# Performance work log

Hardware: AMD Instinct MI355X
Metric: run time of the kernel (lower is better)

The kernel has to match this reference:

```python
import jax, jax.numpy as jnp
import numpy as np

D_IN = 768
D_LATENT = 16384
BATCH = 8192
K = 32


def _xavier(key, shape):
    fan_out, fan_in = shape
    limit = float(np.sqrt(6.0 / (fan_in + fan_out)))
    return jax.random.uniform(key, shape, jnp.float32, -limit, limit)


def setup_inputs() -> dict:
    key = jax.random.key(0)
    k1, k2, k3 = jax.random.split(key, 3)
    x = jax.random.normal(k1, (BATCH, D_IN), dtype=jnp.float32)
    W_enc = _xavier(k2, (D_LATENT, D_IN))   # encoder.weight: [d_latent, d_in]
    W_dec = _xavier(k3, (D_IN, D_LATENT))   # decoder.weight: [d_in, d_latent]
    return {"x": x, "W_enc": W_enc, "W_dec": W_dec, "k": K}


def reference(x, W_enc, W_dec, k):
    # Encoder: Linear (no bias) + ReLU -> z: [B, d_latent]
    z = jax.nn.relu(jnp.einsum('bd,ld->bl', x, W_enc))
    # Per-row top-k mask via scatter of ones at top-k indices
    _, idx = jax.lax.top_k(z, k)                      # idx: [B, k]
    rows = jnp.arange(z.shape[0])[:, None]            # [B, 1]
    mask = jnp.zeros_like(z).at[rows, idx].set(1.0)
    z = z * mask
    # Decoder: Linear (no bias) -> x_hat: [B, d_in]
    x_hat = jnp.einsum('bl,dl->bd', z, W_dec)
    return x_hat, z
```

## Files before the change

kernel.cpp:

```cpp
#include <hip/hip_runtime.h>
#include <hip/hip_bf16.h>
#include <stdint.h>

#define MB 8192
#define NL 16384
#define KD 768
#define TOPK 32
#define CAND_NEED 48
#define TAU 0.70f
#define CAP_MIN 288

typedef short bf16x8 __attribute__((ext_vector_type(8)));
typedef float f32x4 __attribute__((ext_vector_type(4)));
typedef unsigned short ushort_t;

__device__ __forceinline__ short f2bf(float f) {
  unsigned u = __builtin_bit_cast(unsigned, f);
  u = (u + 0x7fffu + ((u >> 16) & 1u)) >> 16;
  return (short)u;
}
__device__ __forceinline__ float bf2f(ushort_t u) {
  return __builtin_bit_cast(float, (unsigned)u << 16);
}

__device__ __forceinline__ void gload16(const ushort_t* g, short* l) {
  __builtin_amdgcn_global_load_lds(
      (const __attribute__((address_space(1))) void*)g,
      (__attribute__((address_space(3))) void*)l, 16, 0, 0);
}

__global__ __launch_bounds__(256) void cvt_bf16(const float* __restrict__ in,
                                                ushort_t* __restrict__ out, int n8) {
  int i = blockIdx.x * 256 + threadIdx.x;
  if (i >= n8) return;
  const float4 v0 = *(const float4*)(in + (size_t)i * 8);
  const float4 v1 = *(const float4*)(in + (size_t)i * 8 + 4);
  bf16x8 p;
  p[0] = f2bf(v0.x); p[1] = f2bf(v0.y); p[2] = f2bf(v0.z); p[3] = f2bf(v0.w);
  p[4] = f2bf(v1.x); p[5] = f2bf(v1.y); p[6] = f2bf(v1.z); p[7] = f2bf(v1.w);
  *(bf16x8*)(out + (size_t)i * 8) = p;
}

__global__ __launch_bounds__(256) void transpose_wdec_pack(const float* __restrict__ W,
                                                           ushort_t* __restrict__ WT) {
  __shared__ float tile[32][33];
  int l0 = blockIdx.x * 32;
  int d0 = blockIdx.y * 32;
  int lx = threadIdx.x;
  for (int i = threadIdx.y; i < 32; i += 8)
    tile[i][lx] = W[(size_t)(d0 + i) * NL + (l0 + lx)];
  __syncthreads();
  int d = d0 + lx;
  int pos = (d < 512) ? ((d & 255) * 2 + (d >> 8)) : d;
  for (int i = threadIdx.y; i < 32; i += 8)
    WT[(size_t)(l0 + i) * KD + pos] = (ushort_t)f2bf(tile[lx][i]);
}

#define GBM 128
#define GBN 128
#define GBK 32
#define LDA 32

__device__ __forceinline__ void emit_cands(const f32x4 (&acc)[4][4], int m0, int n0,
                                           int wr64, int wc64, int er, int ec,
                                           int* __restrict__ cnt,
                                           unsigned* __restrict__ lists, int cap) {
#pragma unroll
  for (int i = 0; i < 4; i++)
#pragma unroll
    for (int j = 0; j < 4; j++)
#pragma unroll
      for (int r = 0; r < 4; r++) {
        float v = acc[i][j][r];
        if (v > TAU) {
          int grow = m0 + wr64 + i * 16 + er + r;
          int gcol = n0 + wc64 + j * 16 + ec;
          int pos = atomicAdd(&cnt[grow], 1);
          if (pos < cap)
            lists[(size_t)grow * cap + pos] =
                (unsigned)gcol | ((unsigned)(ushort_t)f2bf(v) << 16);
        }
      }
}

__global__ __launch_bounds__(256, 4) void encoder_gemm_pre2(const ushort_t* __restrict__ Xb,
                                                            const ushort_t* __restrict__ Wb,
                                                            int* __restrict__ cnt,
                                                            unsigned* __restrict__ lists,
                                                            int cap) {
  __shared__ short Al[2][GBM][LDA];
  __shared__ short Bl[2][GBN][LDA];

  const int tid = threadIdx.x;
  const int NBN = NL / GBN;
  const int GROUP = 8;
  const int NWG = (MB / GBM) * NBN;
  const int CPX = NWG / 8;
  int bid = (blockIdx.x % 8) * CPX + blockIdx.x / 8;
  int group = bid / (GROUP * NBN);
  int rem = bid % (GROUP * NBN);
  int bm = group * GROUP + (rem % GROUP);
  int bn = rem / GROUP;
  const int m0 = bm * GBM, n0 = bn * GBN;

  const int srow = tid >> 2;
  const int slog = (tid & 3) ^ ((tid >> 3) & 3);
  const int w = tid >> 6;

  const ushort_t* Asrc = Xb + (size_t)(m0 + srow) * KD + slog * 8;
  const ushort_t* Bsrc = Wb + (size_t)(n0 + srow) * KD + slog * 8;

#define STAGE(BUF, KT)                                              \
  {                                                                 \
    const int koff_ = (KT) * GBK;                                   \
    short* la_ = &Al[BUF][0][0] + w * 512;                          \
    short* lb_ = &Bl[BUF][0][0] + w * 512;                          \
    gload16(Asrc + koff_, la_);                                     \
    gload16(Asrc + (size_t)64 * KD + koff_, la_ + 2048);            \
    gload16(Bsrc + koff_, lb_);                                     \
    gload16(Bsrc + (size_t)64 * KD + koff_, lb_ + 2048);            \
  }

  const int lane = tid & 63;
  const int wr64 = (w >> 1) * 64;
  const int wc64 = (w & 1) * 64;
  const int fr = lane & 15;
  const int fkb_sw = (((lane >> 4) ^ ((fr >> 1) & 3))) * 8;

  f32x4 acc[4][4];
#pragma unroll
  for (int i = 0; i < 4; i++)
#pragma unroll
    for (int j = 0; j < 4; j++)
#pragma unroll
      for (int r = 0; r < 4; r++) acc[i][j][r] = 0.f;

  STAGE(0, 0);
  STAGE(1, 1);

  const int NT = KD / GBK;
  for (int kt = 0; kt < NT; kt++) {
    if (kt + 1 < NT) {
      asm volatile("s_waitcnt vmcnt(4)" ::: "memory");
    } else {
      asm volatile("s_waitcnt vmcnt(0)" ::: "memory");
    }
    __builtin_amdgcn_s_barrier();

    const int cur = kt & 1;
    bf16x8 af[4], bg[4];
#pragma unroll
    for (int i = 0; i < 4; i++)
      af[i] = *(const bf16x8*)&Al[cur][wr64 + i * 16 + fr][fkb_sw];
#pragma unroll
    for (int j = 0; j < 4; j++)
      bg[j] = *(const bf16x8*)&Bl[cur][wc64 + j * 16 + fr][fkb_sw];

#pragma unroll
    for (int i = 0; i < 4; i++)
#pragma unroll
      for (int j = 0; j < 4; j++)
        acc[i][j] = __builtin_amdgcn_mfma_f32_16x16x32_bf16(af[i], bg[j], acc[i][j], 0, 0, 0);

    __builtin_amdgcn_s_barrier();
    if (kt + 2 < NT) STAGE(cur, kt + 2);
  }

  const int er = (lane >> 4) * 4;
  const int ec = lane & 15;
  emit_cands(acc, m0, n0, wr64, wc64, er, ec, cnt, lists, cap);
#undef STAGE
}

__global__ __launch_bounds__(256, 4) void encoder_gemm_f32(const float* __restrict__ X,
                                                           const float* __restrict__ Wenc,
                                                           int* __restrict__ cnt,
                                                           unsigned* __restrict__ lists,
                                                           int cap) {
  __shared__ short Al[2][GBM][LDA];
  __shared__ short Bl[2][GBN][LDA];

  const int tid = threadIdx.x;
  const int NBN = NL / GBN;
  const int GROUP = 8;
  int bid = blockIdx.x;
  int group = bid / (GROUP * NBN);
  int rem = bid % (GROUP * NBN);
  int bm = group * GROUP + (rem % GROUP);
  int bn = rem / GROUP;
  const int m0 = bm * GBM, n0 = bn * GBN;

  const int srow = tid >> 2;
  const int skg = tid & 3;
  const int sw8 = (skg ^ ((srow >> 1) & 3)) * 8;

  const float* Abase = X + (size_t)(m0 + srow) * KD + skg * 8;
  const float* Bbase = Wenc + (size_t)(n0 + srow) * KD + skg * 8;

  float4 ra0, ra1, ra2, ra3, rb0, rb1, rb2, rb3;

#define FLOADS(KT)                                         \
  {                                                        \
    const float* ap_ = Abase + (KT) * GBK;                 \
    const float* bp_ = Bbase + (KT) * GBK;                 \
    ra0 = *(const float4*)(ap_);                           \
    ra1 = *(const float4*)(ap_ + 4);                       \
    ra2 = *(const float4*)(ap_ + (size_t)64 * KD);         \
    ra3 = *(const float4*)(ap_ + (size_t)64 * KD + 4);     \
    rb0 = *(const float4*)(bp_);                           \
    rb1 = *(const float4*)(bp_ + 4);                       \
    rb2 = *(const float4*)(bp_ + (size_t)64 * KD);         \
    rb3 = *(const float4*)(bp_ + (size_t)64 * KD + 4);     \
  }

#define CVT8(DST, FA, FB)                                                    \
  {                                                                          \
    bf16x8 p_;                                                               \
    p_[0] = f2bf(FA.x); p_[1] = f2bf(FA.y); p_[2] = f2bf(FA.z);              \
    p_[3] = f2bf(FA.w); p_[4] = f2bf(FB.x); p_[5] = f2bf(FB.y);              \
    p_[6] = f2bf(FB.z); p_[7] = f2bf(FB.w);                                  \
    *(bf16x8*)(DST) = p_;                                                    \
  }

#define FWRITE(BUF)                                      \
  {                                                      \
    CVT8(&Al[BUF][srow][sw8], ra0, ra1);                 \
    CVT8(&Al[BUF][srow + 64][sw8], ra2, ra3);            \
    CVT8(&Bl[BUF][srow][sw8], rb0, rb1);                 \
    CVT8(&Bl[BUF][srow + 64][sw8], rb2, rb3);            \
  }

  const int lane = tid & 63;
  const int w = tid >> 6;
  const int wr64 = (w >> 1) * 64;
  const int wc64 = (w & 1) * 64;
  const int fr = lane & 15;
  const int fkb_sw = (((lane >> 4) ^ ((fr >> 1) & 3))) * 8;

  f32x4 acc[4][4];
#pragma unroll
  for (int i = 0; i < 4; i++)
#pragma unroll
    for (int j = 0; j < 4; j++)
#pragma unroll
      for (int r = 0; r < 4; r++) acc[i][j][r] = 0.f;

  FLOADS(0);
  FWRITE(0);
  __syncthreads();

  const int NT = KD / GBK;
  for (int kt = 0; kt < NT; kt++) {
    const int cur = kt & 1;
    if (kt + 1 < NT) FLOADS(kt + 1);

    bf16x8 af[4], bg[4];
#pragma unroll
    for (int i = 0; i < 4; i++)
      af[i] = *(const bf16x8*)&Al[cur][wr64 + i * 16 + fr][fkb_sw];
#pragma unroll
    for (int j = 0; j < 4; j++)
      bg[j] = *(const bf16x8*)&Bl[cur][wc64 + j * 16 + fr][fkb_sw];

#pragma unroll
    for (int i = 0; i < 4; i++)
#pragma unroll
      for (int j = 0; j < 4; j++)
        acc[i][j] = __builtin_amdgcn_mfma_f32_16x16x32_bf16(af[i], bg[j], acc[i][j], 0, 0, 0);

    if (kt + 1 < NT) FWRITE(cur ^ 1);
    __syncthreads();
  }

  const int er = (lane >> 4) * 4;
  const int ec = lane & 15;
  emit_cands(acc, m0, n0, wr64, wc64, er, ec, cnt, lists, cap);
#undef FLOADS
#undef CVT8
#undef FWRITE
}

__global__ __launch_bounds__(256) void select_decode(const int* __restrict__ cnt,
                                                     const unsigned* __restrict__ lists,
                                                     int cap,
                                                     const float* __restrict__ X,
                                                     const float* __restrict__ Wenc,
                                                     const ushort_t* __restrict__ WdTb,
                                                     const float* __restrict__ Wdec,
                                                     int use_wdt,
                                                     float* __restrict__ Z,
                                                     float* __restrict__ Xhat) {
  __shared__ float xrow[KD];
  __shared__ int cj[512];
  __shared__ float cv[512];
  __shared__ int s48_j[CAND_NEED];
  __shared__ float s48_v[CAND_NEED];
  __shared__ int sel_j[TOPK];
  __shared__ float sel_v[TOPK];
  __shared__ float red_v[256];
  __shared__ int red_i[256];

  const int tid = threadIdx.x;
  const int row = blockIdx.x;
  float* z = Z + (size_t)row * NL;

  if (tid < KD / 4)
    ((float4*)xrow)[tid] = ((const float4*)(X + (size_t)row * KD))[tid];

  const int n = cnt[row];
  const bool fb = (n < CAND_NEED) || (n > cap) || (n > 512);

  if (!fb) {
    for (int i = tid; i < n; i += 256) {
      unsigned e = lists[(size_t)row * cap + i];
      cj[i] = (int)(e & 0xffffu);
      cv[i] = bf2f((ushort_t)(e >> 16));
    }
    __syncthreads();
    for (int i = tid; i < n; i += 256) {
      float vi = cv[i];
      int ji = cj[i];
      int r = 0;
      for (int c = 0; c < n; c++) {
        float vc = cv[c];
        r += (int)((vc > vi) || (vc == vi && cj[c] < ji));
      }
      if (r < CAND_NEED) { s48_j[r] = ji; s48_v[r] = vi; }
    }
    __syncthreads();
    if (tid < CAND_NEED) {
      const float4* wr4 = (const float4*)(Wenc + (size_t)s48_j[tid] * KD);
      float s = 0.f;
#pragma unroll 8
      for (int k4 = 0; k4 < KD / 4; k4++) {
        float4 w = wr4[k4];
        s = fmaf(xrow[4 * k4 + 0], w.x, s);
        s = fmaf(xrow[4 * k4 + 1], w.y, s);
        s = fmaf(xrow[4 * k4 + 2], w.z, s);
        s = fmaf(xrow[4 * k4 + 3], w.w, s);
      }
      s48_v[tid] = s;
    } else if (tid >= 64) {
      const f32x4 zf = {0.f, 0.f, 0.f, 0.f};
      f32x4* z4 = (f32x4*)z;
      for (int i = tid - 64; i < NL / 4; i += 192)
        __builtin_nontemporal_store(zf, z4 + i);
    }
    __syncthreads();
    if (tid < CAND_NEED) {
      float vi = s48_v[tid];
      int ji = s48_j[tid];
      int r = 0;
      for (int c = 0; c < CAND_NEED; c++) {
        float vc = s48_v[c];
        r += (int)((vc > vi) || (vc == vi && s48_j[c] < ji));
      }
      if (r < TOPK) { sel_j[r] = ji; sel_v[r] = fmaxf(vi, 0.f); }
    }
    __syncthreads();
    if (tid < TOPK) z[sel_j[tid]] = sel_v[tid];
  } else {
    for (int j = tid; j < NL; j += 256) {
      const float* wr = Wenc + (size_t)j * KD;
      float s = 0.f;
      for (int k = 0; k < KD; k++) s = fmaf(xrow[k], wr[k], s);
      z[j] = fmaxf(s, 0.f);
    }
    __syncthreads();
    for (int t = 0; t < TOPK; t++) {
      float bm = -1.f;
      int bi = NL;
      for (int j = tid; j < NL; j += 256) {
        float v = z[j];
        if (v > bm || (v == bm && j < bi)) { bm = v; bi = j; }
      }
      red_v[tid] = bm;
      red_i[tid] = bi;
      __syncthreads();
      for (int s2 = 128; s2 > 0; s2 >>= 1) {
        if (tid < s2) {
          float v2 = red_v[tid + s2];
          int i2 = red_i[tid + s2];
          if (v2 > red_v[tid] || (v2 == red_v[tid] && i2 < red_i[tid])) {
            red_v[tid] = v2;
            red_i[tid] = i2;
          }
        }
        __syncthreads();
      }
      if (tid == 0) {
        sel_j[t] = red_i[0];
        sel_v[t] = red_v[0];
        z[red_i[0]] = -1.f;
      }
      __syncthreads();
    }
    for (int j = tid; j < NL; j += 256) z[j] = 0.f;
    __syncthreads();
    if (tid < TOPK) z[sel_j[tid]] = sel_v[tid];
  }
  __syncthreads();

  float a00 = 0.f, a01 = 0.f, a02 = 0.f;
  float a10 = 0.f, a11 = 0.f, a12 = 0.f;
  float a20 = 0.f, a21 = 0.f, a22 = 0.f;
  float a30 = 0.f, a31 = 0.f, a32 = 0.f;
  if (use_wdt) {
#define DEC(P0, P1, P2, TT)                                   \
    {                                                         \
      float v = sel_v[TT];                                    \
      const ushort_t* wr = WdTb + (size_t)sel_j[TT] * KD;     \
      unsigned u = ((const unsigned*)wr)[tid];                \
      P0 = fmaf(v, bf2f((ushort_t)(u & 0xffffu)), P0);        \
      P1 = fmaf(v, bf2f((ushort_t)(u >> 16)), P1);            \
      P2 = fmaf(v, bf2f(wr[512 + tid]), P2);                  \
    }
    for (int t = 0; t < TOPK; t += 4) {
      DEC(a00, a01, a02, t)
      DEC(a10, a11, a12, t + 1)
      DEC(a20, a21, a22, t + 2)
      DEC(a30, a31, a32, t + 3)
    }
#undef DEC
  } else {
    for (int t = 0; t < TOPK; t++) {
      float v = sel_v[t];
      const float* wc = Wdec + sel_j[t];
      a00 = fmaf(v, wc[(size_t)tid * NL], a00);
      a01 = fmaf(v, wc[(size_t)(tid + 256) * NL], a01);
      a02 = fmaf(v, wc[(size_t)(tid + 512) * NL], a02);
    }
  }
  float* xo = Xhat + (size_t)row * KD;
  __builtin_nontemporal_store((a00 + a10) + (a20 + a30), xo + tid);
  __builtin_nontemporal_store((a01 + a11) + (a21 + a31), xo + tid + 256);
  __builtin_nontemporal_store((a02 + a12) + (a22 + a32), xo + tid + 512);
}

extern "C" void kernel_launch(void* const* d_in, const int* in_sizes, int n_in,
                              void* d_out, int out_size, void* d_ws, size_t ws_size,
                              hipStream_t stream) {
  const float* x = (const float*)d_in[0];
  const float* Wenc = (const float*)d_in[1];
  const float* Wdec = (const float*)d_in[2];

  float* xhat = (float*)d_out;
  float* z = (float*)d_out + (size_t)MB * KD;

  const size_t cnt_b = (size_t)MB * sizeof(int);
  const size_t wsh_b = (size_t)NL * KD * sizeof(ushort_t);
  const size_t xb_b = (size_t)MB * KD * sizeof(ushort_t);
  const size_t entry = sizeof(unsigned);

  char* ws = (char*)d_ws;
  int* cnt = (int*)ws;
  size_t off = cnt_b;

  int use_pre = 0, use_wdt = 0, cap = 1;
  ushort_t* Wsh = nullptr;
  ushort_t* Xb = nullptr;
  unsigned* lists = nullptr;

  if (ws_size >= cnt_b + wsh_b + xb_b + (size_t)MB * entry * CAP_MIN) {
    use_pre = 1; use_wdt = 1;
    Wsh = (ushort_t*)(ws + off); off += wsh_b;
    Xb = (ushort_t*)(ws + off); off += xb_b;
    lists = (unsigned*)(ws + off);
    size_t c = (ws_size - off) / ((size_t)MB * entry);
    cap = (int)(c > 512 ? 512 : c);
  } else if (ws_size >= cnt_b + wsh_b + (size_t)MB * entry * CAP_MIN) {
    use_wdt = 1;
    Wsh = (ushort_t*)(ws + off); off += wsh_b;
    lists = (unsigned*)(ws + off);
    size_t c = (ws_size - off) / ((size_t)MB * entry);
    cap = (int)(c > 512 ? 512 : c);
  } else {
    lists = (unsigned*)(ws + off);
    size_t avail = (ws_size > off) ? (ws_size - off) : 0;
    size_t c = avail / ((size_t)MB * entry);
    cap = (int)(c > 512 ? 512 : c);
    if (cap < 1) cap = 1;
  }

  hipMemsetAsync(cnt, 0, cnt_b, stream);

  if (use_pre) {
    int nx8 = MB * KD / 8, nw8 = NL * KD / 8;
    cvt_bf16<<<(nx8 + 255) / 256, 256, 0, stream>>>(x, Xb, nx8);
    cvt_bf16<<<(nw8 + 255) / 256, 256, 0, stream>>>(Wenc, Wsh, nw8);
    encoder_gemm_pre2<<<(MB / GBM) * (NL / GBN), 256, 0, stream>>>(Xb, Wsh, cnt, lists, cap);
    dim3 g(NL / 32, KD / 32);
    transpose_wdec_pack<<<g, dim3(32, 8), 0, stream>>>(Wdec, Wsh);
  } else {
    if (use_wdt) {
      dim3 g(NL / 32, KD / 32);
      transpose_wdec_pack<<<g, dim3(32, 8), 0, stream>>>(Wdec, Wsh);
    }
    encoder_gemm_f32<<<(MB / GBM) * (NL / GBN), 256, 0, stream>>>(x, Wenc, cnt, lists, cap);
  }
  select_decode<<<MB, 256, 0, stream>>>(cnt, lists, cap, x, Wenc, Wsh, Wdec, use_wdt,
                                        z, xhat);
}
```

Baseline: 744.9 us.

## Process one row per wavefront in select_decode and drop block barriers

Restructures the select/decode kernel so each 64-lane wavefront handles one row, with four rows per block, instead of a whole 256-thread block per row. Block-wide __syncthreads and the shared-memory reduction are replaced with wave-local execution, shuffle reductions and vmcnt waits. The decoder weight transpose now writes a plain row-major bf16 layout, and each lane produces contiguous output pairs stored as float2. Per-row work is spread over fewer lanes, so the candidate rank sort and the z zeroing run longer per row; the intent is to save on barrier overhead and gain occupancy.

```diff
diff --git a/kernel.cpp b/kernel.cpp
--- a/kernel.cpp
+++ b/kernel.cpp
@@ -12,6 +12,7 @@
 
 typedef short bf16x8 __attribute__((ext_vector_type(8)));
 typedef float f32x4 __attribute__((ext_vector_type(4)));
+typedef float f32x2 __attribute__((ext_vector_type(2)));
 typedef unsigned short ushort_t;
 
 __device__ __forceinline__ short f2bf(float f) {
@@ -41,8 +42,8 @@
   *(bf16x8*)(out + (size_t)i * 8) = p;
 }
 
-__global__ __launch_bounds__(256) void transpose_wdec_pack(const float* __restrict__ W,
-                                                           ushort_t* __restrict__ WT) {
+__global__ __launch_bounds__(256) void transpose_wdec(const float* __restrict__ W,
+                                                      ushort_t* __restrict__ WT) {
   __shared__ float tile[32][33];
   int l0 = blockIdx.x * 32;
   int d0 = blockIdx.y * 32;
@@ -50,10 +51,8 @@
   for (int i = threadIdx.y; i < 32; i += 8)
     tile[i][lx] = W[(size_t)(d0 + i) * NL + (l0 + lx)];
   __syncthreads();
-  int d = d0 + lx;
-  int pos = (d < 512) ? ((d & 255) * 2 + (d >> 8)) : d;
   for (int i = threadIdx.y; i < 32; i += 8)
-    WT[(size_t)(l0 + i) * KD + pos] = (ushort_t)f2bf(tile[lx][i]);
+    WT[(size_t)(l0 + i) * KD + (d0 + lx)] = (ushort_t)f2bf(tile[lx][i]);
 }
 
 #define GBM 128
@@ -290,151 +289,144 @@
                                                      int use_wdt,
                                                      float* __restrict__ Z,
                                                      float* __restrict__ Xhat) {
-  __shared__ float xrow[KD];
-  __shared__ int cj[512];
-  __shared__ float cv[512];
-  __shared__ int s48_j[CAND_NEED];
-  __shared__ float s48_v[CAND_NEED];
-  __shared__ int sel_j[TOPK];
-  __shared__ float sel_v[TOPK];
-  __shared__ float red_v[256];
-  __shared__ int red_i[256];
+  __shared__ float xrow[4][KD];
+  __shared__ int cj[4][512];
+  __shared__ float cv[4][512];
+  __shared__ int s48_j[4][CAND_NEED];
+  __shared__ float s48_v[4][CAND_NEED];
+  __shared__ int sel_j[4][TOPK];
+  __shared__ float sel_v[4][TOPK];
 
   const int tid = threadIdx.x;
-  const int row = blockIdx.x;
+  const int w = tid >> 6;
+  const int lane = tid & 63;
+  const int row = blockIdx.x * 4 + w;
   float* z = Z + (size_t)row * NL;
 
-  if (tid < KD / 4)
-    ((float4*)xrow)[tid] = ((const float4*)(X + (size_t)row * KD))[tid];
+  {
+    const float4* xs = (const float4*)(X + (size_t)row * KD);
+    float4* xd = (float4*)xrow[w];
+#pragma unroll
+    for (int q = 0; q < 3; q++) xd[lane + 64 * q] = xs[lane + 64 * q];
+  }
 
   const int n = cnt[row];
   const bool fb = (n < CAND_NEED) || (n > cap) || (n > 512);
 
   if (!fb) {
-    for (int i = tid; i < n; i += 256) {
+    for (int i = lane; i < n; i += 64) {
       unsigned e = lists[(size_t)row * cap + i];
-      cj[i] = (int)(e & 0xffffu);
-      cv[i] = bf2f((ushort_t)(e >> 16));
-    }
-    __syncthreads();
-    for (int i = tid; i < n; i += 256) {
-      float vi = cv[i];
-      int ji = cj[i];
+      cj[w][i] = (int)(e & 0xffffu);
+      cv[w][i] = bf2f((ushort_t)(e >> 16));
+    }
+    for (int i = lane; i < n; i += 64) {
+      float vi = cv[w][i];
+      int ji = cj[w][i];
       int r = 0;
       for (int c = 0; c < n; c++) {
-        float vc = cv[c];
-        r += (int)((vc > vi) || (vc == vi && cj[c] < ji));
-      }
-      if (r < CAND_NEED) { s48_j[r] = ji; s48_v[r] = vi; }
-    }
-    __syncthreads();
-    if (tid < CAND_NEED) {
-      const float4* wr4 = (const float4*)(Wenc + (size_t)s48_j[tid] * KD);
+        float vc = cv[w][c];
+        r += (int)((vc > vi) || (vc == vi && cj[w][c] < ji));
+      }
+      if (r < CAND_NEED) { s48_j[w][r] = ji; s48_v[w][r] = vi; }
+    }
+    if (lane < CAND_NEED) {
+      const float4* wr4 = (const float4*)(Wenc + (size_t)s48_j[w][lane] * KD);
       float s = 0.f;
 #pragma unroll 8
       for (int k4 = 0; k4 < KD / 4; k4++) {
-        float4 w = wr4[k4];
-        s = fmaf(xrow[4 * k4 + 0], w.x, s);
-        s = fmaf(xrow[4 * k4 + 1], w.y, s);
-        s = fmaf(xrow[4 * k4 + 2], w.z, s);
-        s = fmaf(xrow[4 * k4 + 3], w.w, s);
-      }
-      s48_v[tid] = s;
-    } else if (tid >= 64) {
+        float4 wv = wr4[k4];
+        s = fmaf(xrow[w][4 * k4 + 0], wv.x, s);
+        s = fmaf(xrow[w][4 * k4 + 1], wv.y, s);
+        s = fmaf(xrow[w][4 * k4 + 2], wv.z, s);
+        s = fmaf(xrow[w][4 * k4 + 3], wv.w, s);
+      }
+      s48_v[w][lane] = s;
+    }
+    {
       const f32x4 zf = {0.f, 0.f, 0.f, 0.f};
       f32x4* z4 = (f32x4*)z;
-      for (int i = tid - 64; i < NL / 4; i += 192)
+      for (int i = lane; i < NL / 4; i += 64)
         __builtin_nontemporal_store(zf, z4 + i);
     }
-    __syncthreads();
-    if (tid < CAND_NEED) {
-      float vi = s48_v[tid];
-      int ji = s48_j[tid];
+    if (lane < CAND_NEED) {
+      float vi = s48_v[w][lane];
+      int ji = s48_j[w][lane];
       int r = 0;
       for (int c = 0; c < CAND_NEED; c++) {
-        float vc = s48_v[c];
-        r += (int)((vc > vi) || (vc == vi && s48_j[c] < ji));
-      }
-      if (r < TOPK) { sel_j[r] = ji; sel_v[r] = fmaxf(vi, 0.f); }
-    }
-    __syncthreads();
-    if (tid < TOPK) z[sel_j[tid]] = sel_v[tid];
+        float vc = s48_v[w][c];
+        r += (int)((vc > vi) || (vc == vi && s48_j[w][c] < ji));
+      }
+      if (r < TOPK) { sel_j[w][r] = ji; sel_v[w][r] = fmaxf(vi, 0.f); }
+    }
+    asm volatile("s_waitcnt vmcnt(0)" ::: "memory");
+    if (lane < TOPK) z[sel_j[w][lane]] = sel_v[w][lane];
   } else {
-    for (int j = tid; j < NL; j += 256) {
+    for (int j = lane; j < NL; j += 64) {
       const float* wr = Wenc + (size_t)j * KD;
       float s = 0.f;
-      for (int k = 0; k < KD; k++) s = fmaf(xrow[k], wr[k], s);
+      for (int k = 0; k < KD; k++) s = fmaf(xrow[w][k], wr[k], s);
       z[j] = fmaxf(s, 0.f);
     }
-    __syncthreads();
+    asm volatile("s_waitcnt vmcnt(0)" ::: "memory");
     for (int t = 0; t < TOPK; t++) {
       float bm = -1.f;
       int bi = NL;
-      for (int j = tid; j < NL; j += 256) {
+      for (int j = lane; j < NL; j += 64) {
         float v = z[j];
         if (v > bm || (v == bm && j < bi)) { bm = v; bi = j; }
       }
-      red_v[tid] = bm;
-      red_i[tid] = bi;
-      __syncthreads();
-      for (int s2 = 128; s2 > 0; s2 >>= 1) {
-        if (tid < s2) {
-          float v2 = red_v[tid + s2];
-          int i2 = red_i[tid + s2];
-          if (v2 > red_v[tid] || (v2 == red_v[tid] && i2 < red_i[tid])) {
-            red_v[tid] = v2;
-            red_i[tid] = i2;
-          }
-        }
-        __syncthreads();
-      }
-      if (tid == 0) {
-        sel_j[t] = red_i[0];
-        sel_v[t] = red_v[0];
-        z[red_i[0]] = -1.f;
-      }
-      __syncthreads();
-    }
-    for (int j = tid; j < NL; j += 256) z[j] = 0.f;
-    __syncthreads();
-    if (tid < TOPK) z[sel_j[tid]] = sel_v[tid];
-  }
-  __syncthreads();
-
-  float a00 = 0.f, a01 = 0.f, a02 = 0.f;
-  float a10 = 0.f, a11 = 0.f, a12 = 0.f;
-  float a20 = 0.f, a21 = 0.f, a22 = 0.f;
-  float a30 = 0.f, a31 = 0.f, a32 = 0.f;
+#pragma unroll
+      for (int off = 32; off > 0; off >>= 1) {
+        float vo = __shfl_down(bm, off);
+        int io = __shfl_down(bi, off);
+        if (vo > bm || (vo == bm && io < bi)) { bm = vo; bi = io; }
+      }
+      bm = __shfl(bm, 0);
+      bi = __shfl(bi, 0);
+      if (lane == 0) {
+        sel_j[w][t] = bi;
+        sel_v[w][t] = bm;
+        z[bi] = -1.f;
+      }
+      asm volatile("s_waitcnt vmcnt(0)" ::: "memory");
+    }
+    for (int j = lane; j < NL; j += 64) z[j] = 0.f;
+    asm volatile("s_waitcnt vmcnt(0)" ::: "memory");
+    if (lane < TOPK) z[sel_j[w][lane]] = sel_v[w][lane];
+  }
+
+  float alo[6], ahi[6];
+#pragma unroll
+  for (int q = 0; q < 6; q++) { alo[q] = 0.f; ahi[q] = 0.f; }
   if (use_wdt) {
-#define DEC(P0, P1, P2, TT)                                   \
-    {                                                         \
-      float v = sel_v[TT];                                    \
-      const ushort_t* wr = WdTb + (size_t)sel_j[TT] * KD;     \
-      unsigned u = ((const unsigned*)wr)[tid];                \
-      P0 = fmaf(v, bf2f((ushort_t)(u & 0xffffu)), P0);        \
-      P1 = fmaf(v, bf2f((ushort_t)(u >> 16)), P1);            \
-      P2 = fmaf(v, bf2f(wr[512 + tid]), P2);                  \
-    }
-    for (int t = 0; t < TOPK; t += 4) {
-      DEC(a00, a01, a02, t)
-      DEC(a10, a11, a12, t + 1)
-      DEC(a20, a21, a22, t + 2)
-      DEC(a30, a31, a32, t + 3)
-    }
-#undef DEC
+    for (int t = 0; t < TOPK; t++) {
+      float v = sel_v[w][t];
+      const unsigned* wr = (const unsigned*)(WdTb + (size_t)sel_j[w][t] * KD);
+#pragma unroll
+      for (int q = 0; q < 6; q++) {
+        unsigned u = wr[q * 64 + lane];
+        alo[q] = fmaf(v, bf2f((ushort_t)(u & 0xffffu)), alo[q]);
+        ahi[q] = fmaf(v, bf2f((ushort_t)(u >> 16)), ahi[q]);
+      }
+    }
   } else {
     for (int t = 0; t < TOPK; t++) {
-      float v = sel_v[t];
-      const float* wc = Wdec + sel_j[t];
-      a00 = fmaf(v, wc[(size_t)tid * NL], a00);
-      a01 = fmaf(v, wc[(size_t)(tid + 256) * NL], a01);
-      a02 = fmaf(v, wc[(size_t)(tid + 512) * NL], a02);
+      float v = sel_v[w][t];
+      const float* wc = Wdec + sel_j[w][t];
+#pragma unroll
+      for (int q = 0; q < 6; q++) {
+        int d = q * 128 + lane * 2;
+        alo[q] = fmaf(v, wc[(size_t)d * NL], alo[q]);
+        ahi[q] = fmaf(v, wc[(size_t)(d + 1) * NL], ahi[q]);
+      }
     }
   }
   float* xo = Xhat + (size_t)row * KD;
-  __builtin_nontemporal_store((a00 + a10) + (a20 + a30), xo + tid);
-  __builtin_nontemporal_store((a01 + a11) + (a21 + a31), xo + tid + 256);
-  __builtin_nontemporal_store((a02 + a12) + (a22 + a32), xo + tid + 512);
+#pragma unroll
+  for (int q = 0; q < 6; q++) {
+    f32x2 st = {alo[q], ahi[q]};
+    __builtin_nontemporal_store(st, (f32x2*)(xo + q * 128 + lane * 2));
+  }
 }
 
 extern "C" void kernel_launch(void* const* d_in, const int* in_sizes, int n_in,
@@ -490,14 +482,14 @@
     cvt_bf16<<<(nw8 + 255) / 256, 256, 0, stream>>>(Wenc, Wsh, nw8);
     encoder_gemm_pre2<<<(MB / GBM) * (NL / GBN), 256, 0, stream>>>(Xb, Wsh, cnt, lists, cap);
     dim3 g(NL / 32, KD / 32);
-    transpose_wdec_pack<<<g, dim3(32, 8), 0, stream>>>(Wdec, Wsh);
+    transpose_wdec<<<g, dim3(32, 8), 0, stream>>>(Wdec, Wsh);
   } else {
     if (use_wdt) {
       dim3 g(NL / 32, KD / 32);
-      transpose_wdec_pack<<<g, dim3(32, 8), 0, stream>>>(Wdec, Wsh);
+      transpose_wdec<<<g, dim3(32, 8), 0, stream>>>(Wdec, Wsh);
     }
     encoder_gemm_f32<<<(MB / GBM) * (NL / GBN), 256, 0, stream>>>(x, Wenc, cnt, lists, cap);
   }
-  select_decode<<<MB, 256, 0, stream>>>(cnt, lists, cap, x, Wenc, Wsh, Wdec, use_wdt,
-                                        z, xhat);
-}
+  select_decode<<<MB / 4, 256, 0, stream>>>(cnt, lists, cap, x, Wenc, Wsh, Wdec, use_wdt,
+                                            z, xhat);
+}
```

New measurement: 678.5 us. -8.9%, faster.
